# Kernel optimization log

Hardware: AMD Instinct MI355X
Metric: run time of the kernel (lower is better)

## Reference

```python
import jax, jax.numpy as jnp
from jax import lax
import numpy as np

ALPHA = 100.0  # NetVLAD beta

def _avg_pool2(x):
    # AvgPool2d(2, stride=2) on NCHW
    s = lax.reduce_window(x, 0.0, lax.add, (1, 1, 2, 2), (1, 1, 2, 2), 'VALID')
    return s * 0.25

def _conv3x3(x, w, b):
    y = lax.conv_general_dilated(x, w, (1, 1), 'SAME',
                                 dimension_numbers=('NCHW', 'OIHW', 'NCHW'))
    return y + b[None, :, None, None]

def _l2norm(v, axis):
    return v / jnp.maximum(jnp.linalg.norm(v, axis=axis, keepdims=True), 1e-12)


def setup_inputs() -> dict:
    key = jax.random.key(0)
    ks = jax.random.split(key, 10)
    N, H, W = 16, 512, 512
    K, D = 64, 16          # clusters, NetVLAD feature dim (conv2 out channels)
    T, E, Hd = 64, 300, 512  # caption len, emb dim (rnn_inp=rnn_out), rnn_hid
    img = jax.random.normal(ks[0], (N, 3, H, W), jnp.float32)
    cap = jax.random.normal(ks[1], (N, T, E), jnp.float32)
    conv1_w = jax.random.normal(ks[2], (4, 3, 3, 3), jnp.float32) * 0.1
    conv1_b = jnp.zeros((4,), jnp.float32)
    conv2_w = jax.random.normal(ks[3], (16, 4, 3, 3), jnp.float32) * 0.1
    conv2_b = jnp.zeros((16,), jnp.float32)
    centroids = jax.random.uniform(ks[4], (K, D), jnp.float32)  # torch.rand init
    nv_w = 2.0 * ALPHA * centroids                     # 1x1 conv weight, squeezed [K,D]
    nv_b = -ALPHA * jnp.linalg.norm(centroids, axis=1)  # [K]
    fc_w = jax.random.normal(ks[5], (Hd, K * D), jnp.float32) * 0.02
    fc_b = jnp.zeros((Hd,), jnp.float32)
    hid_w = jax.random.normal(ks[6], (Hd, E + Hd), jnp.float32) * 0.02
    hid_b = jnp.zeros((Hd,), jnp.float32)
    out_w = jax.random.normal(ks[7], (E, Hd), jnp.float32) * 0.02
    out_b = jnp.zeros((E,), jnp.float32)
    return dict(img=img, cap=cap, conv1_w=conv1_w, conv1_b=conv1_b,
                conv2_w=conv2_w, conv2_b=conv2_b, centroids=centroids,
                nv_w=nv_w, nv_b=nv_b, fc_w=fc_w, fc_b=fc_b,
                hid_w=hid_w, hid_b=hid_b, out_w=out_w, out_b=out_b)


def reference(img, cap, conv1_w, conv1_b, conv2_w, conv2_b, centroids,
              nv_w, nv_b, fc_w, fc_b, hid_w, hid_b, out_w, out_b):
    # CNN encoder
    x = jax.nn.relu(_conv3x3(img, conv1_w, conv1_b))
    x = _avg_pool2(x)
    x = jax.nn.relu(_conv3x3(x, conv2_w, conv2_b))
    x = _avg_pool2(x)                      # [N, 16, 128, 128]
    N, C = x.shape[0], x.shape[1]
    xf = x.reshape(N, C, -1)               # [N, C, HW]
    # NetVLAD: 1x1 conv -> softmax over clusters
    soft_assign = jnp.einsum('kc,nch->nkh', nv_w, xf) + nv_b[None, :, None]
    soft_assign = jax.nn.softmax(soft_assign, axis=1)  # [N, K, HW]
    # algebraic two-matmul form of sum_hw a[n,k,hw]*(x[n,c,hw]-centroids[k,c])
    a_sum = soft_assign.sum(axis=-1)                      # [N, K]
    vlad = jnp.einsum('nkh,nch->nkc', soft_assign, xf)    # [N, K, C]
    vlad = vlad - a_sum[:, :, None] * centroids[None]     # [N, K, C]
    vlad = _l2norm(vlad, axis=2)
    vlad = vlad.reshape(N, -1)
    vlad = _l2norm(vlad, axis=1)
    features = vlad @ fc_w.T + fc_b                        # [N, rnn_hid]
    # RNN decoder on sample 0
    feat0 = features[0]
    cap0 = cap[0]                                          # [T, E]

    def step(carry, x_t):
        h, x_in = carry
        comb = jnp.concatenate([x_in, h])
        h_new = jax.nn.sigmoid(hid_w @ comb + hid_b)
        y = jax.nn.sigmoid(out_w @ h_new + out_b)
        return (h_new, x_t), y

    (_, ys) = lax.scan(step, (feat0, cap0[0]), cap0[1:])
    output = jnp.concatenate([cap0[:1], ys], axis=0)       # [T, E]
    loss = jnp.mean((output - cap0) ** 2)
    return loss
```

## Files before the change

### kernel.cpp

```cpp
#include <hip/hip_runtime.h>
#include <math.h>


#define POISON 0xAAAAAAAAu
#define MAGIC  0x13579BDFu

__device__ __forceinline__ float sigmoidf_(float x) {
  return 1.0f / (1.0f + __expf(-x));
}
__device__ __forceinline__ unsigned uld(const unsigned* p) {
  return __hip_atomic_load(p, __ATOMIC_RELAXED, __HIP_MEMORY_SCOPE_AGENT);
}
__device__ __forceinline__ float fld(const float* p) {
  return __hip_atomic_load(p, __ATOMIC_RELAXED, __HIP_MEMORY_SCOPE_AGENT);
}
__device__ __forceinline__ void fst(float* p, float v) {
  __hip_atomic_store(p, v, __ATOMIC_RELAXED, __HIP_MEMORY_SCOPE_AGENT);
}
__device__ __forceinline__ void ust(unsigned* p, unsigned v) {
  __hip_atomic_store(p, v, __ATOMIC_RELAXED, __HIP_MEMORY_SCOPE_AGENT);
}

__global__ __launch_bounds__(256, 1)
void k_fused(const float* __restrict__ img,  const float* __restrict__ cap,
             const float* __restrict__ c1w,  const float* __restrict__ c1b,
             const float* __restrict__ c2w,  const float* __restrict__ c2b,
             const float* __restrict__ cent, const float* __restrict__ nvw,
             const float* __restrict__ nvb,  const float* __restrict__ fcw,
             const float* __restrict__ fcb,  const float* __restrict__ hidw,
             const float* __restrict__ hidb, const float* __restrict__ outw,
             const float* __restrict__ outb,
             float* __restrict__ p1,   float* __restrict__ vacc,
             float* __restrict__ asum, float* __restrict__ feat,
             float* __restrict__ U,    float* __restrict__ H,
             unsigned* __restrict__ flags, float* __restrict__ loss) {
  __shared__ __align__(16) float smem[12832];
  const int bx  = blockIdx.x;
  const int tid = threadIdx.x;
  unsigned* flag_ready = flags + 0;
  unsigned* conv_done  = flags + 1;
  unsigned* vlad_done  = flags + 2;

  if (bx < 8) {
    if (bx == 0) {
      for (int i = tid; i < 1024; i += 256) fst(vacc + i, 0.f);
      if (tid < 64) fst(asum + tid, 0.f);
      if (tid == 0) { fst(loss, 0.f); ust(conv_done, 0u); ust(vlad_done, 0u); }
      unsigned* Uu = (unsigned*)U;
      unsigned* Hu = (unsigned*)H;
      unsigned* Fu = (unsigned*)feat;
      for (int i = tid; i < 63 * 512; i += 256) ust(Uu + i, POISON);
      for (int i = tid; i < 63 * 512; i += 256) ust(Hu + i, POISON);
      if (tid < 256) { ust(Fu + tid, POISON); ust(Fu + tid + 256, POISON); }
      __syncthreads();
      if (tid == 0)
        __hip_atomic_store(flag_ready, MAGIC, __ATOMIC_RELEASE,
                           __HIP_MEMORY_SCOPE_AGENT);
    }
    const int r   = tid >> 2;
    const int cg  = tid & 3;
    const int row = bx * 64 + r;
    float4 wr[32];
    const float4* wp = (const float4*)(hidw + row * 812 + 300 + cg * 128);
    #pragma unroll
    for (int i = 0; i < 32; ++i) wr[i] = wp[i];
    if (bx != 0) {
      if (tid == 0) {
        while (__hip_atomic_load(flag_ready, __ATOMIC_ACQUIRE,
                                 __HIP_MEMORY_SCOPE_AGENT) != MAGIC)
          __builtin_amdgcn_s_sleep(2);
      }
      __syncthreads();
    }
    float* buf0 = smem;
    float* buf1 = smem + 544;
    const int w0 = (tid >> 7) * 136 + (tid & 127);
    const int w1 = ((tid + 256) >> 7) * 136 + ((tid + 256) & 127);
    const int wown = (row >> 7) * 136 + (row & 127);
    const bool own0 = ((tid >> 6) == bx);
    const bool own1 = (((tid + 256) >> 6) == bx);
    {
      const unsigned* fu = (const unsigned*)feat;
      unsigned f0, f1;
      do {
        f0 = uld(fu + tid);
        f1 = uld(fu + tid + 256);
      } while (f0 == POISON || f1 == POISON);
      buf0[w0] = __uint_as_float(f0);
      buf0[w1] = __uint_as_float(f1);
    }
    unsigned upat = 0;
    if (cg == 0) upat = uld((const unsigned*)(U + row));
    __syncthreads();
    unsigned* Hu = (unsigned*)H;
    for (int t = 0; t < 63; ++t) {
      const float* bufc = (t & 1) ? buf1 : buf0;
      const float* rb = bufc + cg * 136;
      float acc = 0.f;
      #pragma unroll
      for (int i = 0; i < 32; ++i) {
        float4 h4 = *(const float4*)(rb + i * 4);
        acc = fmaf(wr[i].x, h4.x, acc);
        acc = fmaf(wr[i].y, h4.y, acc);
        acc = fmaf(wr[i].z, h4.z, acc);
        acc = fmaf(wr[i].w, h4.w, acc);
      }
      acc += __shfl_xor(acc, 1);
      acc += __shfl_xor(acc, 2);
      float hn = 0.f;
      if (cg == 0) {
        while (upat == POISON) upat = uld((const unsigned*)(U + t * 512 + row));
        hn = sigmoidf_(acc + __uint_as_float(upat));
        fst(H + t * 512 + row, hn);
      }
      if (t < 62) {
        float* bufn = (t & 1) ? buf0 : buf1;
        if (cg == 0) {
          bufn[wown] = hn;
          upat = uld((const unsigned*)(U + (t + 1) * 512 + row));
        }
        const unsigned* src = Hu + t * 512;
        unsigned a0 = 0, a1 = 0;
        do {
          if (!own0) a0 = uld(src + tid);
          if (!own1) a1 = uld(src + tid + 256);
        } while ((!own0 && a0 == POISON) || (!own1 && a1 == POISON));
        if (!own0) bufn[w0] = __uint_as_float(a0);
        if (!own1) bufn[w1] = __uint_as_float(a1);
        __syncthreads();
      }
    }
    return;
  }

  if (bx < 71) {
    const int t = bx - 8;
    if (tid == 0) {
      while (__hip_atomic_load(flag_ready, __ATOMIC_ACQUIRE,
                               __HIP_MEMORY_SCOPE_AGENT) != MAGIC)
        __builtin_amdgcn_s_sleep(8);
    }
    __syncthreads();
    float* csh = smem;
    if (tid < 256) csh[tid] = cap[t * 300 + tid];
    if (tid < 44) csh[256 + tid] = cap[t * 300 + 256 + tid];
    __syncthreads();
    #pragma unroll
    for (int rr = 0; rr < 2; ++rr) {
      int rrow = tid + rr * 256;
      float acc = hidb[rrow];
      const float4* w4 = (const float4*)(hidw + rrow * 812);
      const float4* c4 = (const float4*)csh;
      #pragma unroll 5
      for (int i = 0; i < 75; ++i) {
        float4 aa = w4[i]; float4 xx = c4[i];
        acc = fmaf(aa.x, xx.x, acc); acc = fmaf(aa.y, xx.y, acc);
        acc = fmaf(aa.z, xx.z, acc); acc = fmaf(aa.w, xx.w, acc);
      }
      fst(U + t * 512 + rrow, acc);
    }
    __syncthreads();
    const unsigned* Hu = (const unsigned*)H;
    if (tid == 0) {
      while (uld(Hu + (size_t)t * 512) == POISON) __builtin_amdgcn_s_sleep(64);
    }
    __syncthreads();
    float* hsh = smem;
    {
      const unsigned* src = Hu + (size_t)t * 512;
      unsigned a0, a1;
      do {
        a0 = uld(src + tid);
        a1 = uld(src + tid + 256);
      } while (a0 == POISON || a1 == POISON);
      hsh[tid] = __uint_as_float(a0);
      hsh[tid + 256] = __uint_as_float(a1);
    }
    __syncthreads();
    float se = 0.f;
    #pragma unroll
    for (int rr = 0; rr < 2; ++rr) {
      int orow = tid + rr * 256;
      if (orow < 300) {
        float acc = outb[orow];
        const float4* w4 = (const float4*)(outw + orow * 512);
        const float4* h4 = (const float4*)hsh;
        #pragma unroll 4
        for (int i = 0; i < 128; ++i) {
          float4 aa = w4[i]; float4 xx = h4[i];
          acc = fmaf(aa.x, xx.x, acc); acc = fmaf(aa.y, xx.y, acc);
          acc = fmaf(aa.z, xx.z, acc); acc = fmaf(aa.w, xx.w, acc);
        }
        float y = sigmoidf_(acc);
        float d = y - cap[(t + 1) * 300 + orow];
        se = fmaf(d, d, se);
      }
    }
    #pragma unroll
    for (int o = 32; o > 0; o >>= 1) se += __shfl_down(se, o);
    float* red = smem + 512;
    if ((tid & 63) == 0) red[tid >> 6] = se;
    __syncthreads();
    if (tid == 0) {
      float tot = red[0] + red[1] + red[2] + red[3];
      atomicAdd(loss, tot * (1.0f / 19200.0f));
    }
    return;
  }

  if (bx < 79) {
    const int q = bx - 71;
    if (tid == 0) {
      while (uld(vlad_done) != 64u) __builtin_amdgcn_s_sleep(8);
    }
    __syncthreads();
    float* v  = smem;
    float* rn = smem + 1024;
    float* fr = smem + 1088;
    for (int i = tid; i < 1024; i += 256)
      v[i] = fld(vacc + i) - fld(asum + (i >> 4)) * cent[i];
    __syncthreads();
    if (tid < 64) {
      float ss = 0.f;
      #pragma unroll
      for (int c = 0; c < 16; ++c) { float xx = v[tid * 16 + c]; ss = fmaf(xx, xx, ss); }
      rn[tid] = fmaxf(sqrtf(ss), 1e-12f);
    }
    __syncthreads();
    float gs = 0.f;
    for (int i = tid; i < 1024; i += 256) {
      float nv = v[i] / rn[i >> 4];
      v[i] = nv;
      gs = fmaf(nv, nv, gs);
    }
    #pragma unroll
    for (int o = 32; o > 0; o >>= 1) gs += __shfl_down(gs, o);
    if ((tid & 63) == 0) fr[tid >> 6] = gs;
    __syncthreads();
    if (tid == 0) {
      float tot = fr[0] + fr[1] + fr[2] + fr[3];
      fr[8] = 1.0f / fmaxf(sqrtf(tot), 1e-12f);
    }
    __syncthreads();
    float invg = fr[8];
    int row = q * 64 + (tid >> 2);
    int cg = tid & 3;
    float acc = 0.f;
    const float4* fw4 = (const float4*)(fcw + row * 1024 + cg * 256);
    const float4* v4  = (const float4*)(v + cg * 256);
    #pragma unroll 4
    for (int i = 0; i < 64; ++i) {
      float4 aa = fw4[i]; float4 xx = v4[i];
      acc = fmaf(aa.x, xx.x, acc); acc = fmaf(aa.y, xx.y, acc);
      acc = fmaf(aa.z, xx.z, acc); acc = fmaf(aa.w, xx.w, acc);
    }
    acc += __shfl_xor(acc, 1);
    acc += __shfl_xor(acc, 2);
    if (cg == 0) fst(feat + row, fmaf(invg, acc, fcb[row]));
    return;
  }

  if (bx < 143) {
    const int vb = bx - 79;
    float* ps  = smem;
    float* xs  = smem + 8320;
    float* wsh = smem + 10880;
    float* bsh = smem + 11904;
    float* aS  = smem + 11968;
    float* cw  = smem + 12224;
    float* cb  = smem + 12800;
    for (int i = tid; i < 1024; i += 256) wsh[i] = nvw[i];
    if (tid < 64) bsh[tid] = nvb[tid];
    for (int i = tid; i < 576; i += 256) cw[i] = c2w[i];
    if (tid < 16) cb[tid] = c2b[tid];
    if (tid == 0) {
      while (uld(conv_done) != 113u) __builtin_amdgcn_s_sleep(4);
    }
    __syncthreads();
    int ox = tid & 127;
    int oy = vb * 2 + (tid >> 7);
    int y0 = oy * 2 - 1, x0 = ox * 2 - 1;
    float a[16][4];
    #pragma unroll
    for (int oc = 0; oc < 16; ++oc) {
      float bb = cb[oc];
      a[oc][0] = bb; a[oc][1] = bb; a[oc][2] = bb; a[oc][3] = bb;
    }
    #pragma unroll
    for (int ci = 0; ci < 4; ++ci) {
      float P[4][4];
      #pragma unroll
      for (int j = 0; j < 4; ++j) {
        int y = y0 + j;
        #pragma unroll
        for (int i = 0; i < 4; ++i) {
          int x = x0 + i;
          bool ok = ((unsigned)y < 256u) && ((unsigned)x < 256u);
          P[j][i] = ok ? fld(p1 + ci * 65536 + y * 256 + x) : 0.0f;
        }
      }
      #pragma unroll
      for (int oc = 0; oc < 16; ++oc) {
        #pragma unroll
        for (int ky = 0; ky < 3; ++ky) {
          #pragma unroll
          for (int kx = 0; kx < 3; ++kx) {
            float wv = cw[oc * 36 + ci * 9 + ky * 3 + kx];
            a[oc][0] = fmaf(wv, P[ky][kx],         a[oc][0]);
            a[oc][1] = fmaf(wv, P[ky][kx + 1],     a[oc][1]);
            a[oc][2] = fmaf(wv, P[ky + 1][kx],     a[oc][2]);
            a[oc][3] = fmaf(wv, P[ky + 1][kx + 1], a[oc][3]);
          }
        }
      }
    }
    float x[16];
    #pragma unroll
    for (int oc = 0; oc < 16; ++oc)
      x[oc] = 0.25f * (fmaxf(a[oc][0], 0.f) + fmaxf(a[oc][1], 0.f) +
                       fmaxf(a[oc][2], 0.f) + fmaxf(a[oc][3], 0.f));
    float p[64];
    float m = -1e30f;
    #pragma unroll
    for (int k = 0; k < 64; ++k) {
      float acc = bsh[k];
      #pragma unroll
      for (int c = 0; c < 16; ++c) acc = fmaf(wsh[k * 16 + c], x[c], acc);
      p[k] = acc;
      m = fmaxf(m, acc);
    }
    float s = 0.f;
    #pragma unroll
    for (int k = 0; k < 64; ++k) { p[k] = __expf(p[k] - m); s += p[k]; }
    float inv = 1.0f / s;
    #pragma unroll
    for (int k = 0; k < 64; ++k) p[k] *= inv;

    int q = tid >> 6, k = tid & 63;
    float acc[16];
    #pragma unroll
    for (int c = 0; c < 16; ++c) acc[c] = 0.f;
    float accA = 0.f;
    for (int pass = 0; pass < 2; ++pass) {
      __syncthreads();
      if ((tid >> 7) == pass) {
        int tt = tid & 127;
        #pragma unroll
        for (int kk = 0; kk < 64; ++kk) ps[tt * 65 + kk] = p[kk];
        #pragma unroll
        for (int c = 0; c < 16; ++c) xs[tt * 20 + c] = x[c];
      }
      __syncthreads();
      #pragma unroll
      for (int j = 0; j < 32; ++j) {
        int tt = q * 32 + j;
        float pv = ps[tt * 65 + k];
        accA += pv;
        const float4* xv = (const float4*)(xs + tt * 20);
        #pragma unroll
        for (int c4 = 0; c4 < 4; ++c4) {
          float4 xx = xv[c4];
          acc[c4 * 4 + 0] = fmaf(pv, xx.x, acc[c4 * 4 + 0]);
          acc[c4 * 4 + 1] = fmaf(pv, xx.y, acc[c4 * 4 + 1]);
          acc[c4 * 4 + 2] = fmaf(pv, xx.z, acc[c4 * 4 + 2]);
          acc[c4 * 4 + 3] = fmaf(pv, xx.w, acc[c4 * 4 + 3]);
        }
      }
    }
    __syncthreads();
    float* red = ps;
    #pragma unroll
    for (int c = 0; c < 16; ++c) red[tid * 16 + c] = acc[c];
    aS[tid] = accA;
    __syncthreads();
    if (q == 0) {
      float aa = aS[k] + aS[64 + k] + aS[128 + k] + aS[192 + k];
      atomicAdd(&asum[k], aa);
    }
    int k2 = tid >> 2;
    int cgc = (tid & 3) * 4;
    #pragma unroll
    for (int cc = 0; cc < 4; ++cc) {
      int c = cgc + cc;
      float vv = red[(0 * 64 + k2) * 16 + c] + red[(1 * 64 + k2) * 16 + c] +
                 red[(2 * 64 + k2) * 16 + c] + red[(3 * 64 + k2) * 16 + c];
      atomicAdd(&vacc[k2 * 16 + c], vv);
    }
    __syncthreads();
    if (tid == 0)
      __hip_atomic_fetch_add(vlad_done, 1u, __ATOMIC_RELAXED,
                             __HIP_MEMORY_SCOPE_AGENT);
    return;
  }

  {
    const int cbk = bx - 143;
    float* cwsh = smem;
    if (tid < 108) cwsh[tid] = c1w[tid];
    if (tid < 4) cwsh[108 + tid] = c1b[tid];
    __syncthreads();
    for (int o = cbk * 256 + tid; o < 262144; o += 113 * 256) {
      int c  = o >> 16;
      int oy = (o >> 8) & 255;
      int ox = o & 255;
      int y0 = oy * 2 - 1, x0 = ox * 2 - 1;
      float a00, a01, a10, a11;
      a00 = a01 = a10 = a11 = cwsh[108 + c];
      #pragma unroll
      for (int ci = 0; ci < 3; ++ci) {
        float P[4][4];
        #pragma unroll
        for (int j = 0; j < 4; ++j) {
          int y = y0 + j;
          #pragma unroll
          for (int i = 0; i < 4; ++i) {
            int x = x0 + i;
            bool ok = ((unsigned)y < 512u) && ((unsigned)x < 512u);
            P[j][i] = ok ? img[ci * 262144 + y * 512 + x] : 0.0f;
          }
        }
        #pragma unroll
        for (int ky = 0; ky < 3; ++ky) {
          #pragma unroll
          for (int kx = 0; kx < 3; ++kx) {
            float wv = cwsh[c * 27 + ci * 9 + ky * 3 + kx];
            a00 = fmaf(wv, P[ky][kx],         a00);
            a01 = fmaf(wv, P[ky][kx + 1],     a01);
            a10 = fmaf(wv, P[ky + 1][kx],     a10);
            a11 = fmaf(wv, P[ky + 1][kx + 1], a11);
          }
        }
      }
      fst(p1 + o, 0.25f * (fmaxf(a00, 0.f) + fmaxf(a01, 0.f) +
                           fmaxf(a10, 0.f) + fmaxf(a11, 0.f)));
    }
    __syncthreads();
    if (tid == 0) {
      while (__hip_atomic_load(flag_ready, __ATOMIC_ACQUIRE,
                               __HIP_MEMORY_SCOPE_AGENT) != MAGIC)
        __builtin_amdgcn_s_sleep(2);
      __hip_atomic_fetch_add(conv_done, 1u, __ATOMIC_RELAXED,
                             __HIP_MEMORY_SCOPE_AGENT);
    }
  }
}

extern "C" void kernel_launch(void* const* d_in, const int* in_sizes, int n_in,
                              void* d_out, int out_size, void* d_ws, size_t ws_size,
                              hipStream_t stream) {
  (void)in_sizes; (void)n_in; (void)out_size; (void)ws_size;
  const float* img  = (const float*)d_in[0];
  const float* cap  = (const float*)d_in[1];
  const float* c1w  = (const float*)d_in[2];
  const float* c1b  = (const float*)d_in[3];
  const float* c2w  = (const float*)d_in[4];
  const float* c2b  = (const float*)d_in[5];
  const float* cent = (const float*)d_in[6];
  const float* nvw  = (const float*)d_in[7];
  const float* nvb  = (const float*)d_in[8];
  const float* fcw  = (const float*)d_in[9];
  const float* fcb  = (const float*)d_in[10];
  const float* hidw = (const float*)d_in[11];
  const float* hidb = (const float*)d_in[12];
  const float* outw = (const float*)d_in[13];
  const float* outb = (const float*)d_in[14];

  float* ws   = (float*)d_ws;
  float* p1   = ws;
  float* vacc = ws + 262144;
  float* asum = ws + 263168;
  float* feat = ws + 263232;
  float* U    = ws + 263744;
  float* H    = ws + 296000;
  unsigned* flags = (unsigned*)(ws + 328256);

  k_fused<<<256, 256, 0, stream>>>(img, cap, c1w, c1b, c2w, c2b, cent, nvw,
                                   nvb, fcw, fcb, hidw, hidb, outw, outb,
                                   p1, vacc, asum, feat, U, H, flags,
                                   (float*)d_out);
}
```

Baseline: 293.4 us.

## Split fused kernel into front and back kernels, moving RNN scan to second launch

The single persistent kernel is split in two. The first kernel runs the convolutions, the NetVLAD stage, the feature projection and the input-part of the RNN projections, and gives the blocks that used to busy-wait on the recurrence to conv1 (121 conv blocks instead of 113). The second kernel runs the 8-block recurrent scan plus the 63 output/loss blocks, using kernel-boundary ordering instead of poison-flag polling for feat and U. This removes the spinning blocks that occupied CUs during the front work, at the cost of an extra launch and losing overlap between the scan's weight loading and the front stages.

```diff
diff --git a/kernel.cpp b/kernel.cpp
--- a/kernel.cpp
+++ b/kernel.cpp
@@ -22,14 +22,13 @@
 }
 
 __global__ __launch_bounds__(256, 1)
-void k_fused(const float* __restrict__ img,  const float* __restrict__ cap,
+void k_front(const float* __restrict__ img,  const float* __restrict__ cap,
              const float* __restrict__ c1w,  const float* __restrict__ c1b,
              const float* __restrict__ c2w,  const float* __restrict__ c2b,
              const float* __restrict__ cent, const float* __restrict__ nvw,
              const float* __restrict__ nvb,  const float* __restrict__ fcw,
              const float* __restrict__ fcb,  const float* __restrict__ hidw,
-             const float* __restrict__ hidb, const float* __restrict__ outw,
-             const float* __restrict__ outb,
+             const float* __restrict__ hidb,
              float* __restrict__ p1,   float* __restrict__ vacc,
              float* __restrict__ asum, float* __restrict__ feat,
              float* __restrict__ U,    float* __restrict__ H,
@@ -37,119 +36,21 @@
   __shared__ __align__(16) float smem[12832];
   const int bx  = blockIdx.x;
   const int tid = threadIdx.x;
-  unsigned* flag_ready = flags + 0;
+  unsigned* flag_magic = flags + 0;
   unsigned* conv_done  = flags + 1;
   unsigned* vlad_done  = flags + 2;
 
-  if (bx < 8) {
-    if (bx == 0) {
-      for (int i = tid; i < 1024; i += 256) fst(vacc + i, 0.f);
-      if (tid < 64) fst(asum + tid, 0.f);
-      if (tid == 0) { fst(loss, 0.f); ust(conv_done, 0u); ust(vlad_done, 0u); }
-      unsigned* Uu = (unsigned*)U;
-      unsigned* Hu = (unsigned*)H;
-      unsigned* Fu = (unsigned*)feat;
-      for (int i = tid; i < 63 * 512; i += 256) ust(Uu + i, POISON);
-      for (int i = tid; i < 63 * 512; i += 256) ust(Hu + i, POISON);
-      if (tid < 256) { ust(Fu + tid, POISON); ust(Fu + tid + 256, POISON); }
-      __syncthreads();
-      if (tid == 0)
-        __hip_atomic_store(flag_ready, MAGIC, __ATOMIC_RELEASE,
-                           __HIP_MEMORY_SCOPE_AGENT);
-    }
-    const int r   = tid >> 2;
-    const int cg  = tid & 3;
-    const int row = bx * 64 + r;
-    float4 wr[32];
-    const float4* wp = (const float4*)(hidw + row * 812 + 300 + cg * 128);
-    #pragma unroll
-    for (int i = 0; i < 32; ++i) wr[i] = wp[i];
-    if (bx != 0) {
-      if (tid == 0) {
-        while (__hip_atomic_load(flag_ready, __ATOMIC_ACQUIRE,
-                                 __HIP_MEMORY_SCOPE_AGENT) != MAGIC)
-          __builtin_amdgcn_s_sleep(2);
-      }
-      __syncthreads();
-    }
-    float* buf0 = smem;
-    float* buf1 = smem + 544;
-    const int w0 = (tid >> 7) * 136 + (tid & 127);
-    const int w1 = ((tid + 256) >> 7) * 136 + ((tid + 256) & 127);
-    const int wown = (row >> 7) * 136 + (row & 127);
-    const bool own0 = ((tid >> 6) == bx);
-    const bool own1 = (((tid + 256) >> 6) == bx);
-    {
-      const unsigned* fu = (const unsigned*)feat;
-      unsigned f0, f1;
-      do {
-        f0 = uld(fu + tid);
-        f1 = uld(fu + tid + 256);
-      } while (f0 == POISON || f1 == POISON);
-      buf0[w0] = __uint_as_float(f0);
-      buf0[w1] = __uint_as_float(f1);
-    }
-    unsigned upat = 0;
-    if (cg == 0) upat = uld((const unsigned*)(U + row));
-    __syncthreads();
-    unsigned* Hu = (unsigned*)H;
-    for (int t = 0; t < 63; ++t) {
-      const float* bufc = (t & 1) ? buf1 : buf0;
-      const float* rb = bufc + cg * 136;
-      float acc = 0.f;
-      #pragma unroll
-      for (int i = 0; i < 32; ++i) {
-        float4 h4 = *(const float4*)(rb + i * 4);
-        acc = fmaf(wr[i].x, h4.x, acc);
-        acc = fmaf(wr[i].y, h4.y, acc);
-        acc = fmaf(wr[i].z, h4.z, acc);
-        acc = fmaf(wr[i].w, h4.w, acc);
-      }
-      acc += __shfl_xor(acc, 1);
-      acc += __shfl_xor(acc, 2);
-      float hn = 0.f;
-      if (cg == 0) {
-        while (upat == POISON) upat = uld((const unsigned*)(U + t * 512 + row));
-        hn = sigmoidf_(acc + __uint_as_float(upat));
-        fst(H + t * 512 + row, hn);
-      }
-      if (t < 62) {
-        float* bufn = (t & 1) ? buf0 : buf1;
-        if (cg == 0) {
-          bufn[wown] = hn;
-          upat = uld((const unsigned*)(U + (t + 1) * 512 + row));
-        }
-        const unsigned* src = Hu + t * 512;
-        unsigned a0 = 0, a1 = 0;
-        do {
-          if (!own0) a0 = uld(src + tid);
-          if (!own1) a1 = uld(src + tid + 256);
-        } while ((!own0 && a0 == POISON) || (!own1 && a1 == POISON));
-        if (!own0) bufn[w0] = __uint_as_float(a0);
-        if (!own1) bufn[w1] = __uint_as_float(a1);
-        __syncthreads();
-      }
-    }
-    return;
-  }
-
-  if (bx < 71) {
-    const int t = bx - 8;
-    if (tid == 0) {
-      while (__hip_atomic_load(flag_ready, __ATOMIC_ACQUIRE,
-                               __HIP_MEMORY_SCOPE_AGENT) != MAGIC)
-        __builtin_amdgcn_s_sleep(8);
-    }
-    __syncthreads();
+  if (bx < 63) {
+    const int t = bx;
     float* csh = smem;
     if (tid < 256) csh[tid] = cap[t * 300 + tid];
     if (tid < 44) csh[256 + tid] = cap[t * 300 + 256 + tid];
     __syncthreads();
     #pragma unroll
     for (int rr = 0; rr < 2; ++rr) {
-      int rrow = tid + rr * 256;
-      float acc = hidb[rrow];
-      const float4* w4 = (const float4*)(hidw + rrow * 812);
+      int row = tid + rr * 256;
+      float acc = hidb[row];
+      const float4* w4 = (const float4*)(hidw + row * 812);
       const float4* c4 = (const float4*)csh;
       #pragma unroll 5
       for (int i = 0; i < 75; ++i) {
@@ -157,59 +58,13 @@
         acc = fmaf(aa.x, xx.x, acc); acc = fmaf(aa.y, xx.y, acc);
         acc = fmaf(aa.z, xx.z, acc); acc = fmaf(aa.w, xx.w, acc);
       }
-      fst(U + t * 512 + rrow, acc);
-    }
-    __syncthreads();
-    const unsigned* Hu = (const unsigned*)H;
-    if (tid == 0) {
-      while (uld(Hu + (size_t)t * 512) == POISON) __builtin_amdgcn_s_sleep(64);
-    }
-    __syncthreads();
-    float* hsh = smem;
-    {
-      const unsigned* src = Hu + (size_t)t * 512;
-      unsigned a0, a1;
-      do {
-        a0 = uld(src + tid);
-        a1 = uld(src + tid + 256);
-      } while (a0 == POISON || a1 == POISON);
-      hsh[tid] = __uint_as_float(a0);
-      hsh[tid + 256] = __uint_as_float(a1);
-    }
-    __syncthreads();
-    float se = 0.f;
-    #pragma unroll
-    for (int rr = 0; rr < 2; ++rr) {
-      int orow = tid + rr * 256;
-      if (orow < 300) {
-        float acc = outb[orow];
-        const float4* w4 = (const float4*)(outw + orow * 512);
-        const float4* h4 = (const float4*)hsh;
-        #pragma unroll 4
-        for (int i = 0; i < 128; ++i) {
-          float4 aa = w4[i]; float4 xx = h4[i];
-          acc = fmaf(aa.x, xx.x, acc); acc = fmaf(aa.y, xx.y, acc);
-          acc = fmaf(aa.z, xx.z, acc); acc = fmaf(aa.w, xx.w, acc);
-        }
-        float y = sigmoidf_(acc);
-        float d = y - cap[(t + 1) * 300 + orow];
-        se = fmaf(d, d, se);
-      }
-    }
-    #pragma unroll
-    for (int o = 32; o > 0; o >>= 1) se += __shfl_down(se, o);
-    float* red = smem + 512;
-    if ((tid & 63) == 0) red[tid >> 6] = se;
-    __syncthreads();
-    if (tid == 0) {
-      float tot = red[0] + red[1] + red[2] + red[3];
-      atomicAdd(loss, tot * (1.0f / 19200.0f));
+      U[t * 512 + row] = acc;
     }
     return;
   }
 
-  if (bx < 79) {
-    const int q = bx - 71;
+  if (bx < 71) {
+    const int q = bx - 63;
     if (tid == 0) {
       while (uld(vlad_done) != 64u) __builtin_amdgcn_s_sleep(8);
     }
@@ -256,12 +111,12 @@
     }
     acc += __shfl_xor(acc, 1);
     acc += __shfl_xor(acc, 2);
-    if (cg == 0) fst(feat + row, fmaf(invg, acc, fcb[row]));
+    if (cg == 0) feat[row] = fmaf(invg, acc, fcb[row]);
     return;
   }
 
-  if (bx < 143) {
-    const int vb = bx - 79;
+  if (bx < 135) {
+    const int vb = bx - 71;
     float* ps  = smem;
     float* xs  = smem + 8320;
     float* wsh = smem + 10880;
@@ -274,7 +129,7 @@
     for (int i = tid; i < 576; i += 256) cw[i] = c2w[i];
     if (tid < 16) cb[tid] = c2b[tid];
     if (tid == 0) {
-      while (uld(conv_done) != 113u) __builtin_amdgcn_s_sleep(4);
+      while (uld(conv_done) != 121u) __builtin_amdgcn_s_sleep(4);
     }
     __syncthreads();
     int ox = tid & 127;
@@ -394,12 +249,21 @@
   }
 
   {
-    const int cbk = bx - 143;
+    const int cbk = bx - 135;
+    if (cbk == 120) {
+      for (int i = tid; i < 1024; i += 256) fst(vacc + i, 0.f);
+      if (tid < 64) fst(asum + tid, 0.f);
+      if (tid == 0) { fst(loss, 0.f); ust(conv_done, 0u); ust(vlad_done, 0u); }
+      unsigned* Hu = (unsigned*)H;
+      for (int i = tid; i < 63 * 512; i += 256) ust(Hu + i, POISON);
+      __syncthreads();
+      if (tid == 0) ust(flag_magic, MAGIC);
+    }
     float* cwsh = smem;
     if (tid < 108) cwsh[tid] = c1w[tid];
     if (tid < 4) cwsh[108 + tid] = c1b[tid];
     __syncthreads();
-    for (int o = cbk * 256 + tid; o < 262144; o += 113 * 256) {
+    for (int o = cbk * 256 + tid; o < 262144; o += 121 * 256) {
       int c  = o >> 16;
       int oy = (o >> 8) & 255;
       int ox = o & 255;
@@ -436,12 +300,122 @@
     }
     __syncthreads();
     if (tid == 0) {
-      while (__hip_atomic_load(flag_ready, __ATOMIC_ACQUIRE,
-                               __HIP_MEMORY_SCOPE_AGENT) != MAGIC)
-        __builtin_amdgcn_s_sleep(2);
+      while (uld(flag_magic) != MAGIC) __builtin_amdgcn_s_sleep(2);
       __hip_atomic_fetch_add(conv_done, 1u, __ATOMIC_RELAXED,
                              __HIP_MEMORY_SCOPE_AGENT);
     }
+  }
+}
+
+__global__ __launch_bounds__(256, 1)
+void k_back(const float* __restrict__ hidw, const float* __restrict__ U,
+            const float* __restrict__ feat, float* __restrict__ H,
+            const float* __restrict__ outw, const float* __restrict__ outb,
+            const float* __restrict__ cap,  float* __restrict__ loss) {
+  __shared__ __align__(16) float smem[1100];
+  const int bx  = blockIdx.x;
+  const int tid = threadIdx.x;
+  unsigned* Hu = (unsigned*)H;
+
+  if (bx < 8) {
+    const int r   = tid >> 2;
+    const int cg  = tid & 3;
+    const int row = bx * 64 + r;
+    float4 wr[32];
+    const float4* wp = (const float4*)(hidw + row * 812 + 300 + cg * 128);
+    #pragma unroll
+    for (int i = 0; i < 32; ++i) wr[i] = wp[i];
+    float* buf0 = smem;
+    float* buf1 = smem + 544;
+    const int w0 = (tid >> 7) * 136 + (tid & 127);
+    const int w1 = ((tid + 256) >> 7) * 136 + ((tid + 256) & 127);
+    const int wown = (row >> 7) * 136 + (row & 127);
+    const bool own0 = ((tid >> 6) == bx);
+    const bool own1 = (((tid + 256) >> 6) == bx);
+    buf0[w0] = feat[tid];
+    buf0[w1] = feat[tid + 256];
+    __syncthreads();
+    for (int t = 0; t < 63; ++t) {
+      const float* bufc = (t & 1) ? buf1 : buf0;
+      const float* rb = bufc + cg * 136;
+      float uval = (cg == 0) ? U[t * 512 + row] : 0.f;
+      float acc = 0.f;
+      #pragma unroll
+      for (int i = 0; i < 32; ++i) {
+        float4 h4 = *(const float4*)(rb + i * 4);
+        acc = fmaf(wr[i].x, h4.x, acc);
+        acc = fmaf(wr[i].y, h4.y, acc);
+        acc = fmaf(wr[i].z, h4.z, acc);
+        acc = fmaf(wr[i].w, h4.w, acc);
+      }
+      acc += __shfl_xor(acc, 1);
+      acc += __shfl_xor(acc, 2);
+      float hn = 0.f;
+      if (cg == 0) {
+        hn = sigmoidf_(acc + uval);
+        fst(H + t * 512 + row, hn);
+      }
+      if (t < 62) {
+        float* bufn = (t & 1) ? buf0 : buf1;
+        if (cg == 0) bufn[wown] = hn;
+        const unsigned* src = Hu + t * 512;
+        unsigned a0 = 0, a1 = 0;
+        do {
+          if (!own0) a0 = uld(src + tid);
+          if (!own1) a1 = uld(src + tid + 256);
+        } while ((!own0 && a0 == POISON) || (!own1 && a1 == POISON));
+        if (!own0) bufn[w0] = __uint_as_float(a0);
+        if (!own1) bufn[w1] = __uint_as_float(a1);
+        __syncthreads();
+      }
+    }
+    return;
+  }
+
+  const int t = bx - 8;
+  float* hsh = smem;
+  float* red = smem + 512;
+  if (tid == 0) {
+    while (uld(Hu + (size_t)t * 512) == POISON) __builtin_amdgcn_s_sleep(64);
+  }
+  __syncthreads();
+  {
+    const unsigned* src = Hu + (size_t)t * 512;
+    unsigned a0, a1;
+    do {
+      a0 = uld(src + tid);
+      a1 = uld(src + tid + 256);
+    } while (a0 == POISON || a1 == POISON);
+    hsh[tid] = __uint_as_float(a0);
+    hsh[tid + 256] = __uint_as_float(a1);
+  }
+  __syncthreads();
+  float se = 0.f;
+  #pragma unroll
+  for (int rr = 0; rr < 2; ++rr) {
+    int orow = tid + rr * 256;
+    if (orow < 300) {
+      float acc = outb[orow];
+      const float4* w4 = (const float4*)(outw + orow * 512);
+      const float4* h4 = (const float4*)hsh;
+      #pragma unroll 4
+      for (int i = 0; i < 128; ++i) {
+        float4 aa = w4[i]; float4 xx = h4[i];
+        acc = fmaf(aa.x, xx.x, acc); acc = fmaf(aa.y, xx.y, acc);
+        acc = fmaf(aa.z, xx.z, acc); acc = fmaf(aa.w, xx.w, acc);
+      }
+      float y = sigmoidf_(acc);
+      float d = y - cap[(t + 1) * 300 + orow];
+      se = fmaf(d, d, se);
+    }
+  }
+  #pragma unroll
+  for (int o = 32; o > 0; o >>= 1) se += __shfl_down(se, o);
+  if ((tid & 63) == 0) red[tid >> 6] = se;
+  __syncthreads();
+  if (tid == 0) {
+    float tot = red[0] + red[1] + red[2] + red[3];
+    atomicAdd(loss, tot * (1.0f / 19200.0f));
   }
 }
 
@@ -474,8 +448,10 @@
   float* H    = ws + 296000;
   unsigned* flags = (unsigned*)(ws + 328256);
 
-  k_fused<<<256, 256, 0, stream>>>(img, cap, c1w, c1b, c2w, c2b, cent, nvw,
-                                   nvb, fcw, fcb, hidw, hidb, outw, outb,
+  k_front<<<256, 256, 0, stream>>>(img, cap, c1w, c1b, c2w, c2b, cent, nvw,
+                                   nvb, fcw, fcb, hidw, hidb,
                                    p1, vacc, asum, feat, U, H, flags,
                                    (float*)d_out);
-}
+  k_back<<<71, 256, 0, stream>>>(hidw, U, feat, H, outw, outb, cap,
+                                 (float*)d_out);
+}
```

Measured after the change: 292.0 us. Within noise of the previous version (-0.5%).
